# Kernel tuning notes

Hardware: AMD Instinct MI355X
Metric: run time of the kernel (lower is better)

## Reference

```python
import jax, jax.numpy as jnp
import numpy as np

B, N, DIM, H, K = 2, 8192, 256, 8, 32
HD = DIM // H


def setup_inputs() -> dict:
    key = jax.random.key(0)
    ks = jax.random.split(key, 10)
    s = 1.0 / np.sqrt(DIM)
    return {
        "x": jax.random.normal(ks[0], (B, N, DIM), jnp.float32),
        "xyz": jax.random.normal(ks[1], (B, N, 3), jnp.float32),
        "idx": jax.random.randint(ks[2], (B, N, K), 0, N, jnp.int32),
        "Wq": jax.random.normal(ks[3], (DIM, DIM), jnp.float32) * s,
        "bq": jnp.zeros((DIM,), jnp.float32),
        "Wk": jax.random.normal(ks[4], (DIM, DIM), jnp.float32) * s,
        "bk": jnp.zeros((DIM,), jnp.float32),
        "Wv": jax.random.normal(ks[5], (DIM, DIM), jnp.float32) * s,
        "bv": jnp.zeros((DIM,), jnp.float32),
        "Wo": jax.random.normal(ks[6], (DIM, DIM), jnp.float32) * s,
        "bo": jnp.zeros((DIM,), jnp.float32),
        "W1": jax.random.normal(ks[7], (3, 32), jnp.float32) * 0.5,
        "b1": jnp.zeros((32,), jnp.float32),
        "W2": jax.random.normal(ks[8], (32, H), jnp.float32) * 0.2,
        "b2": jnp.zeros((H,), jnp.float32),
    }


def reference(x, xyz, idx, Wq, bq, Wk, bk, Wv, bv, Wo, bo, W1, b1, W2, b2):
    Bn, Nn, C = x.shape
    k = idx.shape[-1]
    q = (x @ Wq + bq).reshape(Bn, Nn, H, HD)          # [B,N,H,hd]
    kf = (x @ Wk + bk).reshape(Bn, Nn, H, HD)
    vf = (x @ Wv + bv).reshape(Bn, Nn, H, HD)
    # gather k neighbors per point (per-batch fancy indexing)
    gather = jax.vmap(lambda f, i: f[i])               # [N,H,hd],[N,k] -> [N,k,H,hd]
    kn = gather(kf, idx)                               # [B,N,k,H,hd]
    vn = gather(vf, idx)
    nxyz = jax.vmap(lambda p, i: p[i])(xyz, idx)       # [B,N,k,3]
    rel = xyz[:, :, None, :] - nxyz                    # [B,N,k,3]
    bias = jax.nn.relu(rel @ W1 + b1) @ W2 + b2        # [B,N,k,H]
    scores = jnp.einsum('bnhd,bnkhd->bnhk', q, kn) / np.sqrt(HD).astype(np.float32)
    scores = scores + bias.transpose(0, 1, 3, 2)       # [B,N,H,k]
    attn = jax.nn.softmax(scores, axis=-1)
    out = jnp.einsum('bnhk,bnkhd->bnhd', attn, vn).reshape(Bn, Nn, C)
    return out @ Wo + bo
```

## Files before the change

### kernel.cpp

```cpp
#include <hip/hip_runtime.h>
#include <hip/hip_bf16.h>

typedef unsigned int uint32;
typedef unsigned short ushort;
typedef __attribute__((ext_vector_type(4))) float floatx4;
typedef __attribute__((ext_vector_type(8))) __bf16 bf16x8;

#define NPTS 8192
#define HSZ 524288

__device__ __forceinline__ ushort f2bf(float f) {
    uint32 u = __float_as_uint(f);
    uint32 r = (u + 0x7fffu + ((u >> 16) & 1u)) >> 16;
    return (ushort)r;
}
__device__ __forceinline__ float bf1(ushort u) { return __uint_as_float((uint32)u << 16); }
__device__ __forceinline__ float bflo(uint32 u) { return __uint_as_float(u << 16); }
__device__ __forceinline__ float bfhi(uint32 u) { return __uint_as_float(u & 0xffff0000u); }

__global__ __launch_bounds__(256) void prep_kernel(
    const float* __restrict__ x, const float* __restrict__ xyz, const int* __restrict__ idx,
    const float* __restrict__ Wq, const float* __restrict__ Wk,
    const float* __restrict__ Wv, const float* __restrict__ Wo,
    const float* __restrict__ bq, const float* __restrict__ bk, const float* __restrict__ bv,
    const float* __restrict__ W1, const float* __restrict__ b1,
    const float* __restrict__ W2, const float* __restrict__ b2,
    ushort* __restrict__ xb, ushort* __restrict__ Wqkvt, ushort* __restrict__ Wot,
    float* __restrict__ biasqkv, ushort* __restrict__ bias_hg) {
    const int bi = blockIdx.x;
    const int tid = threadIdx.x;
    if (bi < 4096) {
        int i = (bi * 256 + tid) * 4;
        float4 v = *(const float4*)(x + i);
        ushort4 o;
        o.x = f2bf(v.x); o.y = f2bf(v.y); o.z = f2bf(v.z); o.w = f2bf(v.w);
        *(ushort4*)(xb + i) = o;
    } else if (bi < 5120) {
        int f = (bi - 4096) * 256 + tid;
        if (f < 768 * 256) {
            int n = f >> 8, k = f & 255;
            int seg = n >> 8, nc = n & 255;
            const float* W = (seg == 0) ? Wq : (seg == 1) ? Wk : Wv;
            Wqkvt[f] = f2bf(W[k * 256 + nc]);
        } else {
            int g = f - 768 * 256;
            int n = g >> 8, k = g & 255;
            Wot[g] = f2bf(Wo[k * 256 + n]);
        }
        if (f < 768) biasqkv[f] = (f < 256) ? bq[f] : (f < 512) ? bk[f - 256] : bv[f - 512];
    } else {
        __shared__ float W1s[96], b1s[32], W2s[256], b2s[8];
        if (tid < 96) W1s[tid] = W1[tid];
        if (tid < 32) b1s[tid] = b1[tid];
        W2s[tid] = W2[tid];
        if (tid < 8) b2s[tid] = b2[tid];
        __syncthreads();
        const int wid = tid >> 6, lane = tid & 63;
        const int s = lane >> 5, j = lane & 31;
        const int p = (bi - 5120) * 8 + wid * 2 + s;
        const int b = p >> 13, n = p & 8191;
        const int nj = idx[(size_t)p * 32 + j];
        const size_t pb = ((size_t)b * NPTS + n) * 3;
        const size_t nb = ((size_t)b * NPTS + nj) * 3;
        const float rx = xyz[pb + 0] - xyz[nb + 0];
        const float ry = xyz[pb + 1] - xyz[nb + 1];
        const float rz = xyz[pb + 2] - xyz[nb + 2];
        float acc[8];
#pragma unroll
        for (int h = 0; h < 8; ++h) acc[h] = b2s[h];
#pragma unroll
        for (int u = 0; u < 32; ++u) {
            float hv = rx * W1s[u] + ry * W1s[32 + u] + rz * W1s[64 + u] + b1s[u];
            hv = fmaxf(hv, 0.f);
#pragma unroll
            for (int h = 0; h < 8; ++h) acc[h] += hv * W2s[u * 8 + h];
        }
#pragma unroll
        for (int h = 0; h < 8; ++h) bias_hg[(size_t)h * HSZ + p * 32 + j] = f2bf(acc[h]);
    }
}

__global__ __launch_bounds__(256) void gemm_qkv(const ushort* __restrict__ A,
                                                const ushort* __restrict__ Wt,
                                                const float* __restrict__ bias,
                                                ushort* __restrict__ qh, ushort* __restrict__ kh,
                                                ushort* __restrict__ vh) {
    __shared__ __align__(16) ushort As[128 * 64];
    __shared__ __align__(16) ushort Bs[128 * 64];
    const int tid = threadIdx.x;
    const int w = tid >> 6, lane = tid & 63;
    const int m0 = blockIdx.y * 128, n0 = blockIdx.x * 128;
    const int wm = (w & 1) * 64, wn = (w >> 1) * 64;

    floatx4 acc[4][4] = {};

    for (int kt = 0; kt < 256; kt += 64) {
        __syncthreads();
#pragma unroll
        for (int c4 = 0; c4 < 4; ++c4) {
            const int c = w * 4 + c4;
            const int r = c * 8 + (lane >> 3);
            const int gseg = (lane & 7) ^ (r & 7);
            const char* ga = (const char*)(A + (size_t)(m0 + r) * 256 + kt) + gseg * 16;
            const char* gb = (const char*)(Wt + (size_t)(n0 + r) * 256 + kt) + gseg * 16;
            __builtin_amdgcn_global_load_lds((const __attribute__((address_space(1))) void*)ga,
                                             (__attribute__((address_space(3))) void*)((char*)As + c * 1024),
                                             16, 0, 0);
            __builtin_amdgcn_global_load_lds((const __attribute__((address_space(1))) void*)gb,
                                             (__attribute__((address_space(3))) void*)((char*)Bs + c * 1024),
                                             16, 0, 0);
        }
        __syncthreads();

        bf16x8 af[2][4], bg[2][4];
#pragma unroll
        for (int kk = 0; kk < 2; ++kk) {
            const int s = kk * 4 + (lane >> 4);
            const int phys = s ^ (lane & 7);
#pragma unroll
            for (int i = 0; i < 4; ++i) {
                af[kk][i] = *(const bf16x8*)((const char*)As + (wm + i * 16 + (lane & 15)) * 128 + phys * 16);
                bg[kk][i] = *(const bf16x8*)((const char*)Bs + (wn + i * 16 + (lane & 15)) * 128 + phys * 16);
            }
        }
#pragma unroll
        for (int kk = 0; kk < 2; ++kk)
#pragma unroll
            for (int mi = 0; mi < 4; ++mi)
#pragma unroll
                for (int ni = 0; ni < 4; ++ni)
                    acc[mi][ni] = __builtin_amdgcn_mfma_f32_16x16x32_bf16(af[kk][mi], bg[kk][ni], acc[mi][ni], 0, 0, 0);
    }

#pragma unroll
    for (int ni = 0; ni < 4; ++ni) {
        const int col = n0 + wn + ni * 16 + (lane & 15);
        const int seg = col >> 8;
        const int head = (col >> 5) & 7;
        const int dim = col & 31;
        ushort* segp = (seg == 0) ? qh : (seg == 1) ? kh : vh;
        const float bv = bias[col];
#pragma unroll
        for (int mi = 0; mi < 4; ++mi) {
            const int row0 = m0 + wm + mi * 16 + (lane >> 4) * 4;
#pragma unroll
            for (int r = 0; r < 4; ++r)
                segp[(size_t)head * HSZ + (size_t)(row0 + r) * 32 + dim] = f2bf(acc[mi][ni][r] + bv);
        }
    }
}

__global__ __launch_bounds__(256) void gemm_mfma64(const ushort* __restrict__ A,
                                                   const ushort* __restrict__ Wt,
                                                   const float* __restrict__ bias,
                                                   float* __restrict__ outv, int N) {
    __shared__ __align__(16) ushort As[64 * 32];
    __shared__ __align__(16) ushort Bs[64 * 32];
    const int tid = threadIdx.x;
    const int w = tid >> 6, lane = tid & 63;
    const int m0 = blockIdx.y * 64, n0 = blockIdx.x * 64;
    const int row = tid >> 2;
    const int col16 = (tid & 3) * 16;

    floatx4 acc[4] = {};

    for (int kt = 0; kt < 256; kt += 32) {
        __syncthreads();
        {
            const char* ga = (const char*)(A + (size_t)(m0 + row) * 256 + kt) + col16;
            const char* gb = (const char*)(Wt + (size_t)(n0 + row) * 256 + kt) + col16;
            __builtin_amdgcn_global_load_lds((const __attribute__((address_space(1))) void*)ga,
                                             (__attribute__((address_space(3))) void*)((char*)As + w * 1024),
                                             16, 0, 0);
            __builtin_amdgcn_global_load_lds((const __attribute__((address_space(1))) void*)gb,
                                             (__attribute__((address_space(3))) void*)((char*)Bs + w * 1024),
                                             16, 0, 0);
        }
        __syncthreads();

        bf16x8 af = *(const bf16x8*)&As[(w * 16 + (lane & 15)) * 32 + (lane >> 4) * 8];
        bf16x8 bg[4];
#pragma unroll
        for (int ni = 0; ni < 4; ++ni)
            bg[ni] = *(const bf16x8*)&Bs[(ni * 16 + (lane & 15)) * 32 + (lane >> 4) * 8];
#pragma unroll
        for (int ni = 0; ni < 4; ++ni)
            acc[ni] = __builtin_amdgcn_mfma_f32_16x16x32_bf16(af, bg[ni], acc[ni], 0, 0, 0);
    }

#pragma unroll
    for (int ni = 0; ni < 4; ++ni) {
        const int col = n0 + ni * 16 + (lane & 15);
        const float bv = bias[col];
        const int row0 = m0 + w * 16 + (lane >> 4) * 4;
#pragma unroll
        for (int r = 0; r < 4; ++r)
            outv[(size_t)(row0 + r) * N + col] = acc[ni][r] + bv;
    }
}

__global__ __launch_bounds__(256) void attn_kernel(
    const ushort* __restrict__ qh, const ushort* __restrict__ kh, const ushort* __restrict__ vh,
    const int* __restrict__ idx, const ushort* __restrict__ bias_hg, ushort* __restrict__ out) {
    const int tid = threadIdx.x, wid = tid >> 6, lane = tid & 63;
    const int h = blockIdx.x >> 11;
    const int pg = blockIdx.x & 2047;
    const int pbase = pg * 8 + wid * 2;

    const char* kh_h = (const char*)(kh + (size_t)h * HSZ);
    const char* vh_h = (const char*)(vh + (size_t)h * HSZ);

    const int s = lane >> 5;
    const int q4 = lane & 3, g = (lane >> 2) & 7;
    const int p = pbase + s;
    const int b = p >> 13;

    const int4 nidx = *(const int4*)(idx + (size_t)p * 32 + g * 4);
    const uint4 qp = *(const uint4*)(qh + (size_t)h * HSZ + p * 32 + q4 * 8);
    const ushort4 bs4 = *(const ushort4*)(bias_hg + (size_t)h * HSZ + p * 32 + g * 4);

    uint32 addr_r[4];
    addr_r[0] = (uint32)(nidx.x + b * NPTS) * 64u + q4 * 16;
    addr_r[1] = (uint32)(nidx.y + b * NPTS) * 64u + q4 * 16;
    addr_r[2] = (uint32)(nidx.z + b * NPTS) * 64u + q4 * 16;
    addr_r[3] = (uint32)(nidx.w + b * NPTS) * 64u + q4 * 16;

    uint4 kreg[4], vreg[4];
#pragma unroll
    for (int i = 0; i < 4; ++i) kreg[i] = *(const uint4*)(kh_h + addr_r[i]);
#pragma unroll
    for (int i = 0; i < 4; ++i) vreg[i] = *(const uint4*)(vh_h + addr_r[i]);

    const float4 qa = {bflo(qp.x), bfhi(qp.x), bflo(qp.y), bfhi(qp.y)};
    const float4 qb = {bflo(qp.z), bfhi(qp.z), bflo(qp.w), bfhi(qp.w)};

    float e_r[4];
    float esum = 0.f;
#pragma unroll
    for (int i = 0; i < 4; ++i) {
        const uint4 kv = kreg[i];
        float d = bflo(kv.x) * qa.x + bfhi(kv.x) * qa.y
                + bflo(kv.y) * qa.z + bfhi(kv.y) * qa.w
                + bflo(kv.z) * qb.x + bfhi(kv.z) * qb.y
                + bflo(kv.w) * qb.z + bfhi(kv.w) * qb.w;
        d += __shfl_xor(d, 1, 64);
        d += __shfl_xor(d, 2, 64);
        const ushort bu = (i == 0) ? bs4.x : (i == 1) ? bs4.y : (i == 2) ? bs4.z : bs4.w;
        const float sc = d * 0.17677669529663687f + bf1(bu);
        const float e = __expf(sc);
        e_r[i] = e;
        esum += e;
    }
    float ssum = esum;
    ssum += __shfl_xor(ssum, 4, 64);
    ssum += __shfl_xor(ssum, 8, 64);
    ssum += __shfl_xor(ssum, 16, 64);
    const float rinv = __builtin_amdgcn_rcpf(ssum);

    {
        float a0 = 0.f, a1 = 0.f, a2 = 0.f, a3 = 0.f, a4 = 0.f, a5 = 0.f, a6 = 0.f, a7 = 0.f;
#pragma unroll
        for (int i = 0; i < 4; ++i) {
            const float wgt = e_r[i];
            const uint4 v = vreg[i];
            a0 += wgt * bflo(v.x); a1 += wgt * bfhi(v.x);
            a2 += wgt * bflo(v.y); a3 += wgt * bfhi(v.y);
            a4 += wgt * bflo(v.z); a5 += wgt * bfhi(v.z);
            a6 += wgt * bflo(v.w); a7 += wgt * bfhi(v.w);
        }
        const bool hi4 = (lane & 4) != 0;
        {
            float t0 = hi4 ? a0 : a4, t1 = hi4 ? a1 : a5, t2 = hi4 ? a2 : a6, t3 = hi4 ? a3 : a7;
            float k0 = hi4 ? a4 : a0, k1 = hi4 ? a5 : a1, k2 = hi4 ? a6 : a2, k3 = hi4 ? a7 : a3;
            a0 = k0 + __shfl_xor(t0, 4, 64);
            a1 = k1 + __shfl_xor(t1, 4, 64);
            a2 = k2 + __shfl_xor(t2, 4, 64);
            a3 = k3 + __shfl_xor(t3, 4, 64);
        }
        const bool hi8 = (lane & 8) != 0;
        {
            float t0 = hi8 ? a0 : a2, t1 = hi8 ? a1 : a3;
            float k0 = hi8 ? a2 : a0, k1 = hi8 ? a3 : a1;
            a0 = k0 + __shfl_xor(t0, 8, 64);
            a1 = k1 + __shfl_xor(t1, 8, 64);
        }
        const bool hi16 = (lane & 16) != 0;
        {
            float t0 = hi16 ? a0 : a1;
            float k0 = hi16 ? a1 : a0;
            a0 = k0 + __shfl_xor(t0, 16, 64);
        }
        const uint32 u = (uint32)f2bf(a0 * rinv);
        const uint32 up = (uint32)__shfl_xor((int)u, 16, 64);
        if (!hi16) {
            const int D = q4 * 8 + (hi4 ? 4 : 0) + (hi8 ? 2 : 0);
            *(uint32*)(out + (size_t)p * 256 + h * 32 + D) = u | (up << 16);
        }
    }
}

extern "C" void kernel_launch(void* const* d_in, const int* in_sizes, int n_in,
                              void* d_out, int out_size, void* d_ws, size_t ws_size,
                              hipStream_t stream) {
    const float* x   = (const float*)d_in[0];
    const float* xyz = (const float*)d_in[1];
    const int*   idx = (const int*)d_in[2];
    const float* Wq = (const float*)d_in[3];
    const float* bq = (const float*)d_in[4];
    const float* Wk = (const float*)d_in[5];
    const float* bk = (const float*)d_in[6];
    const float* Wv = (const float*)d_in[7];
    const float* bv = (const float*)d_in[8];
    const float* Wo = (const float*)d_in[9];
    const float* bo = (const float*)d_in[10];
    const float* W1 = (const float*)d_in[11];
    const float* b1 = (const float*)d_in[12];
    const float* W2 = (const float*)d_in[13];
    const float* b2 = (const float*)d_in[14];

    char* wsb = (char*)d_ws;
    ushort* x_bf    = (ushort*)wsb;
    ushort* aout_bf = x_bf;
    ushort* qh      = (ushort*)(wsb + 8388608);
    ushort* kh      = (ushort*)(wsb + 16777216);
    ushort* vh      = (ushort*)(wsb + 25165824);
    ushort* bias_hg = (ushort*)(wsb + 33554432);
    ushort* Wqkvt   = (ushort*)(wsb + 41943040);
    ushort* Wot     = (ushort*)(wsb + 42336256);
    float*  biasqkv = (float*)(wsb + 42467328);

    prep_kernel<<<7168, 256, 0, stream>>>(x, xyz, idx, Wq, Wk, Wv, Wo, bq, bk, bv,
                                          W1, b1, W2, b2, x_bf, Wqkvt, Wot, biasqkv, bias_hg);

    gemm_qkv<<<dim3(6, 128), 256, 0, stream>>>(x_bf, Wqkvt, biasqkv, qh, kh, vh);

    attn_kernel<<<16384, 256, 0, stream>>>(qh, kh, vh, idx, bias_hg, aout_bf);

    gemm_mfma64<<<dim3(4, 256), 256, 0, stream>>>(aout_bf, Wot, bo, (float*)d_out, 256);
}
```

Baseline: 174.0 us.

## Interleave K and V per head and give each thread eight neighbors in attention

The QKV GEMM now writes K and V into one interleaved per-head buffer with 128-byte rows (K in the first 64 bytes, V in the second), so each gathered neighbor row brings in both K and V from one contiguous region. The attention kernel is remapped so each 16-lane group handles one point and each thread covers eight neighbors instead of four. This halves the block count and removes one shuffle level in both the softmax sum and the output reduction. It aims to cut scattered gather traffic and reduction overhead, at the cost of more registers per thread and a more branchy epilogue in the GEMM.

```diff
diff --git a/kernel.cpp b/kernel.cpp
--- a/kernel.cpp
+++ b/kernel.cpp
@@ -8,6 +8,7 @@
 
 #define NPTS 8192
 #define HSZ 524288
+#define HSZ2 1048576
 
 __device__ __forceinline__ ushort f2bf(float f) {
     uint32 u = __float_as_uint(f);
@@ -83,8 +84,8 @@
 __global__ __launch_bounds__(256) void gemm_qkv(const ushort* __restrict__ A,
                                                 const ushort* __restrict__ Wt,
                                                 const float* __restrict__ bias,
-                                                ushort* __restrict__ qh, ushort* __restrict__ kh,
-                                                ushort* __restrict__ vh) {
+                                                ushort* __restrict__ qh,
+                                                ushort* __restrict__ kvh) {
     __shared__ __align__(16) ushort As[128 * 64];
     __shared__ __align__(16) ushort Bs[128 * 64];
     const int tid = threadIdx.x;
@@ -137,15 +138,20 @@
         const int col = n0 + wn + ni * 16 + (lane & 15);
         const int seg = col >> 8;
         const int head = (col >> 5) & 7;
-        const int dim = col & 31;
-        ushort* segp = (seg == 0) ? qh : (seg == 1) ? kh : vh;
+        const int dim = (col & 31) + ((seg == 2) ? 32 : 0);
         const float bv = bias[col];
 #pragma unroll
         for (int mi = 0; mi < 4; ++mi) {
             const int row0 = m0 + wm + mi * 16 + (lane >> 4) * 4;
 #pragma unroll
-            for (int r = 0; r < 4; ++r)
-                segp[(size_t)head * HSZ + (size_t)(row0 + r) * 32 + dim] = f2bf(acc[mi][ni][r] + bv);
+            for (int r = 0; r < 4; ++r) {
+                const int row = row0 + r;
+                const ushort val = f2bf(acc[mi][ni][r] + bv);
+                if (seg == 0)
+                    qh[(size_t)head * HSZ + (size_t)row * 32 + dim] = val;
+                else
+                    kvh[(size_t)head * HSZ2 + (size_t)row * 64 + dim] = val;
+            }
         }
     }
 }
@@ -200,44 +206,49 @@
 }
 
 __global__ __launch_bounds__(256) void attn_kernel(
-    const ushort* __restrict__ qh, const ushort* __restrict__ kh, const ushort* __restrict__ vh,
+    const ushort* __restrict__ qh, const ushort* __restrict__ kvh,
     const int* __restrict__ idx, const ushort* __restrict__ bias_hg, ushort* __restrict__ out) {
     const int tid = threadIdx.x, wid = tid >> 6, lane = tid & 63;
-    const int h = blockIdx.x >> 11;
-    const int pg = blockIdx.x & 2047;
-    const int pbase = pg * 8 + wid * 2;
-
-    const char* kh_h = (const char*)(kh + (size_t)h * HSZ);
-    const char* vh_h = (const char*)(vh + (size_t)h * HSZ);
-
-    const int s = lane >> 5;
-    const int q4 = lane & 3, g = (lane >> 2) & 7;
+    const int h = blockIdx.x >> 10;
+    const int pg = blockIdx.x & 1023;
+    const int pbase = pg * 16 + wid * 4;
+
+    const char* kv_h = (const char*)(kvh + (size_t)h * HSZ2);
+
+    const int s = lane >> 4;
+    const int g = (lane >> 2) & 3, q4 = lane & 3;
     const int p = pbase + s;
     const int b = p >> 13;
 
-    const int4 nidx = *(const int4*)(idx + (size_t)p * 32 + g * 4);
+    const int4 n0 = *(const int4*)(idx + (size_t)p * 32 + g * 8);
+    const int4 n1 = *(const int4*)(idx + (size_t)p * 32 + g * 8 + 4);
     const uint4 qp = *(const uint4*)(qh + (size_t)h * HSZ + p * 32 + q4 * 8);
-    const ushort4 bs4 = *(const ushort4*)(bias_hg + (size_t)h * HSZ + p * 32 + g * 4);
-
-    uint32 addr_r[4];
-    addr_r[0] = (uint32)(nidx.x + b * NPTS) * 64u + q4 * 16;
-    addr_r[1] = (uint32)(nidx.y + b * NPTS) * 64u + q4 * 16;
-    addr_r[2] = (uint32)(nidx.z + b * NPTS) * 64u + q4 * 16;
-    addr_r[3] = (uint32)(nidx.w + b * NPTS) * 64u + q4 * 16;
-
-    uint4 kreg[4], vreg[4];
-#pragma unroll
-    for (int i = 0; i < 4; ++i) kreg[i] = *(const uint4*)(kh_h + addr_r[i]);
-#pragma unroll
-    for (int i = 0; i < 4; ++i) vreg[i] = *(const uint4*)(vh_h + addr_r[i]);
+    const uint4 bs = *(const uint4*)(bias_hg + (size_t)h * HSZ + p * 32 + g * 8);
+
+    const uint32 roff = (uint32)(b * NPTS);
+    uint32 addr[8];
+    addr[0] = ((uint32)n0.x + roff) * 128u + q4 * 16;
+    addr[1] = ((uint32)n0.y + roff) * 128u + q4 * 16;
+    addr[2] = ((uint32)n0.z + roff) * 128u + q4 * 16;
+    addr[3] = ((uint32)n0.w + roff) * 128u + q4 * 16;
+    addr[4] = ((uint32)n1.x + roff) * 128u + q4 * 16;
+    addr[5] = ((uint32)n1.y + roff) * 128u + q4 * 16;
+    addr[6] = ((uint32)n1.z + roff) * 128u + q4 * 16;
+    addr[7] = ((uint32)n1.w + roff) * 128u + q4 * 16;
+
+    uint4 kreg[8], vreg[8];
+#pragma unroll
+    for (int i = 0; i < 8; ++i) kreg[i] = *(const uint4*)(kv_h + addr[i]);
+#pragma unroll
+    for (int i = 0; i < 8; ++i) vreg[i] = *(const uint4*)(kv_h + addr[i] + 64);
 
     const float4 qa = {bflo(qp.x), bfhi(qp.x), bflo(qp.y), bfhi(qp.y)};
     const float4 qb = {bflo(qp.z), bfhi(qp.z), bflo(qp.w), bfhi(qp.w)};
 
-    float e_r[4];
+    float e_r[8];
     float esum = 0.f;
 #pragma unroll
-    for (int i = 0; i < 4; ++i) {
+    for (int i = 0; i < 8; ++i) {
         const uint4 kv = kreg[i];
         float d = bflo(kv.x) * qa.x + bfhi(kv.x) * qa.y
                 + bflo(kv.y) * qa.z + bfhi(kv.y) * qa.w
@@ -245,58 +256,46 @@
                 + bflo(kv.w) * qb.z + bfhi(kv.w) * qb.w;
         d += __shfl_xor(d, 1, 64);
         d += __shfl_xor(d, 2, 64);
-        const ushort bu = (i == 0) ? bs4.x : (i == 1) ? bs4.y : (i == 2) ? bs4.z : bs4.w;
-        const float sc = d * 0.17677669529663687f + bf1(bu);
-        const float e = __expf(sc);
+        const uint32 bw = (i < 2) ? bs.x : (i < 4) ? bs.y : (i < 6) ? bs.z : bs.w;
+        const float bb = (i & 1) ? bfhi(bw) : bflo(bw);
+        const float e = __expf(d * 0.17677669529663687f + bb);
         e_r[i] = e;
         esum += e;
     }
     float ssum = esum;
     ssum += __shfl_xor(ssum, 4, 64);
     ssum += __shfl_xor(ssum, 8, 64);
-    ssum += __shfl_xor(ssum, 16, 64);
     const float rinv = __builtin_amdgcn_rcpf(ssum);
 
+    float a0 = 0.f, a1 = 0.f, a2 = 0.f, a3 = 0.f, a4 = 0.f, a5 = 0.f, a6 = 0.f, a7 = 0.f;
+#pragma unroll
+    for (int i = 0; i < 8; ++i) {
+        const float wgt = e_r[i];
+        const uint4 v = vreg[i];
+        a0 += wgt * bflo(v.x); a1 += wgt * bfhi(v.x);
+        a2 += wgt * bflo(v.y); a3 += wgt * bfhi(v.y);
+        a4 += wgt * bflo(v.z); a5 += wgt * bfhi(v.z);
+        a6 += wgt * bflo(v.w); a7 += wgt * bfhi(v.w);
+    }
+    const bool hi4 = (lane & 4) != 0;
     {
-        float a0 = 0.f, a1 = 0.f, a2 = 0.f, a3 = 0.f, a4 = 0.f, a5 = 0.f, a6 = 0.f, a7 = 0.f;
-#pragma unroll
-        for (int i = 0; i < 4; ++i) {
-            const float wgt = e_r[i];
-            const uint4 v = vreg[i];
-            a0 += wgt * bflo(v.x); a1 += wgt * bfhi(v.x);
-            a2 += wgt * bflo(v.y); a3 += wgt * bfhi(v.y);
-            a4 += wgt * bflo(v.z); a5 += wgt * bfhi(v.z);
-            a6 += wgt * bflo(v.w); a7 += wgt * bfhi(v.w);
-        }
-        const bool hi4 = (lane & 4) != 0;
-        {
-            float t0 = hi4 ? a0 : a4, t1 = hi4 ? a1 : a5, t2 = hi4 ? a2 : a6, t3 = hi4 ? a3 : a7;
-            float k0 = hi4 ? a4 : a0, k1 = hi4 ? a5 : a1, k2 = hi4 ? a6 : a2, k3 = hi4 ? a7 : a3;
-            a0 = k0 + __shfl_xor(t0, 4, 64);
-            a1 = k1 + __shfl_xor(t1, 4, 64);
-            a2 = k2 + __shfl_xor(t2, 4, 64);
-            a3 = k3 + __shfl_xor(t3, 4, 64);
-        }
-        const bool hi8 = (lane & 8) != 0;
-        {
-            float t0 = hi8 ? a0 : a2, t1 = hi8 ? a1 : a3;
-            float k0 = hi8 ? a2 : a0, k1 = hi8 ? a3 : a1;
-            a0 = k0 + __shfl_xor(t0, 8, 64);
-            a1 = k1 + __shfl_xor(t1, 8, 64);
-        }
-        const bool hi16 = (lane & 16) != 0;
-        {
-            float t0 = hi16 ? a0 : a1;
-            float k0 = hi16 ? a1 : a0;
-            a0 = k0 + __shfl_xor(t0, 16, 64);
-        }
-        const uint32 u = (uint32)f2bf(a0 * rinv);
-        const uint32 up = (uint32)__shfl_xor((int)u, 16, 64);
-        if (!hi16) {
-            const int D = q4 * 8 + (hi4 ? 4 : 0) + (hi8 ? 2 : 0);
-            *(uint32*)(out + (size_t)p * 256 + h * 32 + D) = u | (up << 16);
-        }
-    }
+        float t0 = hi4 ? a0 : a4, t1 = hi4 ? a1 : a5, t2 = hi4 ? a2 : a6, t3 = hi4 ? a3 : a7;
+        float k0 = hi4 ? a4 : a0, k1 = hi4 ? a5 : a1, k2 = hi4 ? a6 : a2, k3 = hi4 ? a7 : a3;
+        a0 = k0 + __shfl_xor(t0, 4, 64);
+        a1 = k1 + __shfl_xor(t1, 4, 64);
+        a2 = k2 + __shfl_xor(t2, 4, 64);
+        a3 = k3 + __shfl_xor(t3, 4, 64);
+    }
+    const bool hi8 = (lane & 8) != 0;
+    {
+        float t0 = hi8 ? a0 : a2, t1 = hi8 ? a1 : a3;
+        float k0 = hi8 ? a2 : a0, k1 = hi8 ? a3 : a1;
+        a0 = k0 + __shfl_xor(t0, 8, 64);
+        a1 = k1 + __shfl_xor(t1, 8, 64);
+    }
+    const int D = q4 * 8 + (hi4 ? 4 : 0) + (hi8 ? 2 : 0);
+    const uint32 u = (uint32)f2bf(a0 * rinv) | ((uint32)f2bf(a1 * rinv) << 16);
+    *(uint32*)(out + (size_t)p * 256 + h * 32 + D) = u;
 }
 
 extern "C" void kernel_launch(void* const* d_in, const int* in_sizes, int n_in,
@@ -322,8 +321,7 @@
     ushort* x_bf    = (ushort*)wsb;
     ushort* aout_bf = x_bf;
     ushort* qh      = (ushort*)(wsb + 8388608);
-    ushort* kh      = (ushort*)(wsb + 16777216);
-    ushort* vh      = (ushort*)(wsb + 25165824);
+    ushort* kvh     = (ushort*)(wsb + 16777216);
     ushort* bias_hg = (ushort*)(wsb + 33554432);
     ushort* Wqkvt   = (ushort*)(wsb + 41943040);
     ushort* Wot     = (ushort*)(wsb + 42336256);
@@ -332,9 +330,9 @@
     prep_kernel<<<7168, 256, 0, stream>>>(x, xyz, idx, Wq, Wk, Wv, Wo, bq, bk, bv,
                                           W1, b1, W2, b2, x_bf, Wqkvt, Wot, biasqkv, bias_hg);
 
-    gemm_qkv<<<dim3(6, 128), 256, 0, stream>>>(x_bf, Wqkvt, biasqkv, qh, kh, vh);
-
-    attn_kernel<<<16384, 256, 0, stream>>>(qh, kh, vh, idx, bias_hg, aout_bf);
+    gemm_qkv<<<dim3(6, 128), 256, 0, stream>>>(x_bf, Wqkvt, biasqkv, qh, kvh);
+
+    attn_kernel<<<8192, 256, 0, stream>>>(qh, kvh, idx, bias_hg, aout_bf);
 
     gemm_mfma64<<<dim3(4, 256), 256, 0, stream>>>(aout_bf, Wot, bo, (float*)d_out, 256);
 }
```

New measurement: 174.0 us. About the same (-0.0%).
